# Kernel tuning notes

Measured on AMD Instinct MI355X. Metric: run time of the kernel, lower is better.

Reference implementation:

```python
import jax, jax.numpy as jnp
import numpy as np
import math

BS, CS, CT, H, W, HID = 32, 640, 768, 24, 24, 64
NUM_ITERS, REG = 50, 0.1


def setup_inputs() -> dict:
    key = jax.random.key(0)
    k1, k2, k3, k4, k5, k6 = jax.random.split(key, 6)
    feat_s = jax.random.normal(k1, (BS, CS, H, W), dtype=jnp.float32)
    feat_t = jax.random.normal(k2, (BS, CT, H, W), dtype=jnp.float32)
    Ws = jax.random.normal(k3, (HID, CS), dtype=jnp.float32) * (1.0 / math.sqrt(CS))
    bs = jax.random.normal(k4, (HID,), dtype=jnp.float32) * 0.01
    Wt = jax.random.normal(k5, (HID, CT), dtype=jnp.float32) * (1.0 / math.sqrt(CT))
    bt = jax.random.normal(k6, (HID,), dtype=jnp.float32) * 0.01
    return {"feat_s": feat_s, "feat_t": feat_t, "Ws": Ws, "bs": bs, "Wt": Wt, "bt": bt}


def _l2norm_dim1(x, eps=1e-12):
    # F.normalize(x, p=2, dim=1) on [BS, N, hid]: normalize over the TOKEN axis (dim=1)
    n = jnp.sqrt(jnp.sum(x * x, axis=1, keepdims=True))
    return x / jnp.maximum(n, eps)


def _log_otp_solver(log_a, log_b, M, num_iters, reg):
    Ms = M / reg  # [BS, N_s, N_t]
    u0 = jnp.zeros_like(log_a)
    v0 = jnp.zeros_like(log_b)

    def step(carry, _):
        u, v = carry
        u = log_a - jax.nn.logsumexp(Ms + v[:, None, :], axis=2)
        v = log_b - jax.nn.logsumexp(Ms + u[:, :, None], axis=1)
        return (u, v), None

    (u, v), _ = jax.lax.scan(step, (u0, v0), None, length=num_iters)
    return Ms + u[:, :, None] + v[:, None, :]


def _forward(feat_s, feat_t, Ws, bs, Wt, bt):
    B, Cs, h, w = feat_s.shape
    Ns = h * w
    B, Ct, ht, wt = feat_t.shape
    Nt = ht * wt
    xs = feat_s.reshape(B, Cs, Ns).transpose(0, 2, 1)  # [B, Ns, Cs]
    xt = feat_t.reshape(B, Ct, Nt).transpose(0, 2, 1)  # [B, Nt, Ct]
    # Linear + L2Norm(dim=1)
    xs = _l2norm_dim1(jnp.einsum('bnc,hc->bnh', xs, Ws) + bs)  # [B, Ns, hid]
    xt = _l2norm_dim1(jnp.einsum('bnc,hc->bnh', xt, Wt) + bt)  # [B, Nt, hid]
    # squared euclidean pairwise distances (cdist p=2, squared)
    sq_s = jnp.sum(xs * xs, axis=-1)  # [B, Ns]
    sq_t = jnp.sum(xt * xt, axis=-1)  # [B, Nt]
    dots = jnp.einsum('bnh,bmh->bnm', xs, xt)  # [B, Ns, Nt]
    M = jnp.maximum(sq_s[:, :, None] + sq_t[:, None, :] - 2.0 * dots, 0.0)
    log_a = jnp.full((B, Ns), -math.log(Ns), dtype=M.dtype)
    log_b = jnp.full((B, Nt), -math.log(Nt), dtype=M.dtype)
    log_T = _log_otp_solver(log_a, log_b, M, NUM_ITERS, REG)
    T = jnp.exp(log_T)
    return jnp.sum(T * M) / B


def reference(feat_s, feat_t, Ws, bs, Wt, bt):
    return _forward(feat_s, feat_t, Ws, bs, Wt, bt)
```

## Files before the change

### kernel.cpp

```cpp
#include <hip/hip_runtime.h>
#include <hip/hip_fp16.h>

#define BSZ 32
#define CS_ 640
#define CT_ 768
#define NTOK 576
#define HID 64
#define ITERS 50
#define WGB 8
#define ROWS 72
#define NWG (BSZ*WGB)
#define MPITCH 640
#define XPITCH 68

#define LOG2_N 9.169925001442312f
#define INV_N 0.001736111111111111f
#define MS_SCALE 14.426950408889634f
#define M_FROM_MSP 0.06931471805599453f

#define OFF_CNT 0
#define OFF_DONE 2048
#define OFF_GSUM 2056
#define OFF_DUMMY 2112
#define OFF_SQP 4160
#define OFF_PACC 151616
#define OFF_XS 299072
#define OFF_XT 2658368

#define L_MS 0
#define L_U 92160
#define L_V 92448
#define L_RED 95008
#define L_EUH 95072
#define L_MROW 95232
#define L_EWH 95520
#define L_UNION 96800
#define SMEM_BYTES 114048

typedef _Float16 half8 __attribute__((ext_vector_type(8)));
typedef _Float16 h2f __attribute__((ext_vector_type(2)));
typedef float f32x4 __attribute__((ext_vector_type(4)));

#if defined(__has_builtin)
#if __has_builtin(__builtin_amdgcn_fdot2)
#define HAVE_FDOT2 1
#endif
#endif

__device__ __forceinline__ float fdot2f(h2f a, h2f b, float c) {
#ifdef HAVE_FDOT2
    return __builtin_amdgcn_fdot2(a, b, c, false);
#else
    return fmaf((float)a[0], (float)b[0], fmaf((float)a[1], (float)b[1], c));
#endif
}

#define APITCH 40

template <int C>
__device__ __forceinline__ void proj_mfma(
    const float* __restrict__ feat,
    const float* __restrict__ W,
    const float* __restrict__ bias,
    __half* __restrict__ out,
    float* __restrict__ sqp,
    _Float16* lA, _Float16* lB, int nblk)
{
    const int tid = threadIdx.x;
    const int lane = tid & 63;
    const int wv = tid >> 6;
    const int n0 = nblk * 64;
    const int fr = lane & 15;
    const int kg = lane >> 4;

    f32x4 acc[4];
#pragma unroll
    for (int n = 0; n < 4; n++) acc[n] = (f32x4){0.f, 0.f, 0.f, 0.f};

    for (int c0 = 0; c0 < C; c0 += 32) {
        __syncthreads();
#pragma unroll
        for (int q = 0; q < 8; q++) {
            int idx = tid + q * 256;
            int t = idx & 63, c = idx >> 6;
            lA[t * APITCH + c] = (_Float16)feat[(size_t)(c0 + c) * NTOK + n0 + t];
        }
#pragma unroll
        for (int q = 0; q < 8; q++) {
            int idx = tid + q * 256;
            int c = idx & 31, h = idx >> 5;
            lB[h * APITCH + c] = (_Float16)W[(size_t)h * C + c0 + c];
        }
        __syncthreads();
        half8 a = *(const half8*)&lA[(wv * 16 + fr) * APITCH + kg * 8];
#pragma unroll
        for (int n = 0; n < 4; n++) {
            half8 b = *(const half8*)&lB[(n * 16 + fr) * APITCH + kg * 8];
            acc[n] = __builtin_amdgcn_mfma_f32_16x16x32_f16(a, b, acc[n], 0, 0, 0);
        }
    }

    __syncthreads();
    float* sred = (float*)lA;
#pragma unroll
    for (int n = 0; n < 4; n++) {
        const int h = n * 16 + fr;
        const float bv = bias[h];
        float s = 0.f;
#pragma unroll
        for (int reg = 0; reg < 4; reg++) {
            const int tok = wv * 16 + kg * 4 + reg;
            float val = acc[n][reg] + bv;
            out[(size_t)(n0 + tok) * HID + h] = __float2half(val);
            s = fmaf(val, val, s);
        }
        s += __shfl_xor(s, 16, 64);
        s += __shfl_xor(s, 32, 64);
        if (lane < 16) sred[wv * 64 + h] = s;
    }
    __syncthreads();
    if (tid < 64)
        sqp[tid] = sred[tid] + sred[64 + tid] + sred[128 + tid] + sred[192 + tid];
}

__global__ __launch_bounds__(256, 4) void k1_proj(
    const float* __restrict__ feat_s, const float* __restrict__ feat_t,
    const float* __restrict__ Ws, const float* __restrict__ bs,
    const float* __restrict__ Wt, const float* __restrict__ bt,
    __half* __restrict__ xs, __half* __restrict__ xt,
    float* __restrict__ sqpart, float* __restrict__ Pacc,
    int* __restrict__ counters, int* __restrict__ done, float* __restrict__ gsum)
{
    __shared__ __align__(16) _Float16 lA[64 * APITCH];
    __shared__ __align__(16) _Float16 lB[64 * APITCH];
    const int nblk = blockIdx.x, b = blockIdx.y, st = blockIdx.z;
    const int tid = threadIdx.x;

    if (st == 0 && nblk < 8) {
        float* pz = Pacc + (size_t)b * NTOK + nblk * 72;
        if (tid < 72) { pz[tid] = 0.f; pz[(size_t)BSZ * NTOK + tid] = 0.f; }
    }
    if (st == 1 && nblk == 0) {
        if (tid < 16) counters[b * 16 + tid] = 0;
        if (b == 0) {
            if (tid == 16) done[0] = 0;
            if (tid == 17) done[1] = 0;
            if (tid == 18) gsum[0] = 0.f;
        }
    }

    if (st == 0) {
        proj_mfma<CS_>(feat_s + (size_t)b * CS_ * NTOK, Ws, bs,
                       xs + (size_t)b * NTOK * HID,
                       sqpart + ((size_t)b * 9 + nblk) * 64, lA, lB, nblk);
    } else {
        proj_mfma<CT_>(feat_t + (size_t)b * CT_ * NTOK, Wt, bt,
                       xt + (size_t)b * NTOK * HID,
                       sqpart + ((size_t)(BSZ + b) * 9 + nblk) * 64, lA, lB, nblk);
    }
}

__global__ __launch_bounds__(1024, 8) void k4_sinkhorn(
    const __half* __restrict__ xsh, const __half* __restrict__ xth,
    const float* __restrict__ sqpart, float* __restrict__ Pacc,
    int* __restrict__ counters, int* __restrict__ done,
    float* __restrict__ gsum, float* __restrict__ dummyout,
    float* __restrict__ out)
{
    extern __shared__ char smem[];
    __half* Ms  = (__half*)(smem + L_MS);
    _Float16* MsH = (_Float16*)(smem + L_MS);
    float* u_l  = (float*)(smem + L_U);
    float* vlg  = (float*)(smem + L_V);
    float* red  = (float*)(smem + L_RED);
    _Float16* eu_h = (_Float16*)(smem + L_EUH);
    float* mrow = (float*)(smem + L_MROW);
    _Float16* ewh = (_Float16*)(smem + L_EWH);
    float* vtmp = (float*)(smem + L_UNION);
    float* ssc  = (float*)(smem + L_UNION);
    float* stc  = (float*)(smem + L_UNION + 256);
    float* sqs  = (float*)(smem + L_UNION + 512);
    float* sqt  = (float*)(smem + L_UNION + 800);
    __half* xs_l = (__half*)(smem + L_UNION + 3104);
    __half* xt_l = (__half*)(smem + L_UNION + 12896);

    const int tid = threadIdx.x;
    const int b = blockIdx.x & 31, part = blockIdx.x >> 5;
    const int r0 = part * ROWS;
    const int lane = tid & 63, wv = tid >> 6;
    float s_kept = 0.f;

    if (tid < 64) {
        const float* sp = sqpart + (size_t)b * 9 * 64 + tid;
        float s = 0.f;
#pragma unroll
        for (int k = 0; k < 9; k++) s += sp[k * 64];
        ssc[tid] = 1.0f / fmaxf(sqrtf(s), 1e-12f);
    } else if (tid < 128) {
        const float* sp = sqpart + (size_t)(BSZ + b) * 9 * 64 + (tid - 64);
        float s = 0.f;
#pragma unroll
        for (int k = 0; k < 9; k++) s += sp[k * 64];
        stc[tid - 64] = 1.0f / fmaxf(sqrtf(s), 1e-12f);
    }
    for (int m = tid; m < MPITCH; m += 1024) ewh[m] = (m < NTOK) ? (_Float16)1.0f : (_Float16)0.0f;
    __syncthreads();

    for (int idx = tid; idx < ROWS * 64; idx += 1024) {
        int r = idx >> 6, h = idx & 63;
        xs_l[r * XPITCH + h] =
            __float2half(__half2float(xsh[((size_t)b * NTOK + r0 + r) * 64 + h]) * ssc[h]);
    }
    if (tid < NTOK) {
        const __half* tp = xth + ((size_t)b * NTOK + tid) * 64;
        float s = 0.f;
#pragma unroll
        for (int h = 0; h < 64; h++) { float v = __half2float(tp[h]) * stc[h]; s = fmaf(v, v, s); }
        sqt[tid] = s;
    }
    __syncthreads();
    if (tid < ROWS) {
        float s = 0.f;
#pragma unroll
        for (int h = 0; h < 64; h++) { float v = __half2float(xs_l[tid * XPITCH + h]); s = fmaf(v, v, s); }
        sqs[tid] = s;
    }

    for (int c0 = 0; c0 < NTOK; c0 += 32) {
        __syncthreads();
        for (int idx = tid; idx < 32 * 64; idx += 1024) {
            int m = idx >> 6, h = idx & 63;
            xt_l[m * XPITCH + h] =
                __float2half(__half2float(xth[((size_t)b * NTOK + c0 + m) * 64 + h]) * stc[h]);
        }
        __syncthreads();
        for (int idx = tid; idx < ROWS * 32; idx += 1024) {
            int r = idx >> 5, c = idx & 31;
            const __half2* xr = (const __half2*)(xs_l + r * XPITCH);
            const __half2* tr = (const __half2*)(xt_l + c * XPITCH);
            float d = 0.f;
#pragma unroll
            for (int h2 = 0; h2 < 32; h2++) {
                float2 av = __half22float2(xr[h2]);
                float2 tv = __half22float2(tr[h2]);
                d = fmaf(av.x, tv.x, d);
                d = fmaf(av.y, tv.y, d);
            }
            float M = fmaxf(sqs[r] + sqt[c] - 2.f * d, 0.f);
            Ms[r * MPITCH + c0 + c] = __float2half(M * MS_SCALE);
        }
    }
    __syncthreads();
    for (int idx = tid; idx < ROWS * (MPITCH - NTOK); idx += 1024) {
        int r = idx >> 6, k = idx & 63;
        Ms[r * MPITCH + NTOK + k] = __float2half(-1000.f);
    }
    __syncthreads();

    for (int r = wv; r < ROWS; r += 16) {
        __half* row = Ms + r * MPITCH;
        float2 f[5];
        float mx = 0.f;
#pragma unroll
        for (int j = 0; j < 5; j++) {
            f[j] = __half22float2(*(const __half2*)&row[128 * j + 2 * lane]);
            mx = fmaxf(mx, fmaxf(f[j].x, f[j].y));
        }
#pragma unroll
        for (int off = 32; off > 0; off >>= 1) mx = fmaxf(mx, __shfl_xor(mx, off, 64));
        if (lane == 0) mrow[r] = mx;
#pragma unroll
        for (int j = 0; j < 5; j++) {
            *(__half2*)&row[128 * j + 2 * lane] = __floats2half2_rn(
                __builtin_amdgcn_exp2f(f[j].x - mx), __builtin_amdgcn_exp2f(f[j].y - mx));
        }
    }
    __syncthreads();

    int* flags = counters + b * 16;

    for (int it = 1; it <= ITERS; ++it) {
        if (it > 1) {
            if (tid < NTOK) {
                const int qr = (it - 1) & 1, qw = it & 1;
                float s = __hip_atomic_load(&Pacc[(size_t)(qr * BSZ + b) * NTOK + tid],
                                            __ATOMIC_RELAXED, __HIP_MEMORY_SCOPE_AGENT);
                ewh[tid] = (_Float16)(INV_N * __builtin_amdgcn_rcpf(s));
                if (tid >= r0 && tid < r0 + ROWS) {
                    if (s_kept != 0.f)
                        (void)__hip_atomic_fetch_add(
                            &Pacc[(size_t)(qw * BSZ + b) * NTOK + tid], -s_kept,
                            __ATOMIC_RELAXED, __HIP_MEMORY_SCOPE_AGENT);
                    s_kept = s;
                }
            }
            __syncthreads();
        }
        h2f vrh[5];
#pragma unroll
        for (int j = 0; j < 5; j++) vrh[j] = *(const h2f*)&ewh[128 * j + 2 * lane];
        for (int r = wv; r < ROWS; r += 16) {
            const _Float16* row = MsH + r * MPITCH;
            float a = 0.f;
#pragma unroll
            for (int j = 0; j < 5; j++)
                a = fdot2f(*(const h2f*)&row[128 * j + 2 * lane], vrh[j], a);
#pragma unroll
            for (int off = 32; off > 0; off >>= 1) a += __shfl_xor(a, off, 64);
            if (lane == 0) {
                eu_h[r] = (_Float16)(INV_N * __builtin_amdgcn_rcpf(a));
                u_l[r] = -LOG2_N - __builtin_amdgcn_logf(a);
            }
        }
        __syncthreads();
        if (tid < 864) {
            int q = tid / 288, p = tid - q * 288;
            const _Float16* col = MsH + 2 * p;
            float a0 = 0.f, a1 = 0.f;
            int n1 = q * 24;
#pragma unroll
            for (int nn = 0; nn < 12; nn++, n1 += 2) {
                uint ea = *(const uint*)&col[n1 * MPITCH];
                uint eb = *(const uint*)&col[(n1 + 1) * MPITCH];
                h2f up = *(const h2f*)&eu_h[n1];
                uint xpk = __builtin_amdgcn_perm(eb, ea, 0x05040100u);
                uint ypk = __builtin_amdgcn_perm(eb, ea, 0x07060302u);
                a0 = fdot2f(__builtin_bit_cast(h2f, xpk), up, a0);
                a1 = fdot2f(__builtin_bit_cast(h2f, ypk), up, a1);
            }
            ((float2*)(vtmp + q * NTOK))[p] = make_float2(a0, a1);
        }
        __syncthreads();
        if (tid < NTOK) {
            float s = vtmp[tid] + vtmp[NTOK + tid] + vtmp[2 * NTOK + tid];
            (void)__hip_atomic_fetch_add(&Pacc[(size_t)((it & 1) * BSZ + b) * NTOK + tid], s,
                                         __ATOMIC_RELAXED, __HIP_MEMORY_SCOPE_AGENT);
        }
        __syncthreads();
        if (tid < WGB) {
            if (tid == part)
                __hip_atomic_store(&flags[tid], it, __ATOMIC_RELAXED, __HIP_MEMORY_SCOPE_AGENT);
            while (__hip_atomic_load(&flags[tid], __ATOMIC_RELAXED, __HIP_MEMORY_SCOPE_AGENT) < it)
                __builtin_amdgcn_s_sleep(1);
        }
        __syncthreads();
    }

    if (tid < NTOK) {
        float s = __hip_atomic_load(&Pacc[(size_t)b * NTOK + tid],
                                    __ATOMIC_RELAXED, __HIP_MEMORY_SCOPE_AGENT);
        vlg[tid] = -LOG2_N - __builtin_amdgcn_logf(s);
    }
    __syncthreads();
    float acc = 0.f;
    for (int idx = tid; idx < ROWS * NTOK; idx += 1024) {
        int r = idx / NTOK, m = idx - r * NTOK;
        float e = __half2float(Ms[r * MPITCH + m]);
        if (e > 0.f) {
            float msp = __builtin_amdgcn_logf(e) + mrow[r];
            acc = fmaf(__builtin_amdgcn_exp2f(u_l[r] + vlg[m]) * e, msp, acc);
        }
    }
#pragma unroll
    for (int off = 32; off > 0; off >>= 1) acc += __shfl_xor(acc, off, 64);
    if (lane == 0) red[wv] = acc;
    __syncthreads();
    if (tid == 0) {
        float s = 0.f;
#pragma unroll
        for (int w2 = 0; w2 < 16; w2++) s += red[w2];
        float old = __hip_atomic_fetch_add(gsum, s * M_FROM_MSP,
                                           __ATOMIC_RELAXED, __HIP_MEMORY_SCOPE_AGENT);
        int* dptr = done + ((old == -1.2345678e33f) ? 1 : 0);
        int prev = __hip_atomic_fetch_add(dptr, 1, __ATOMIC_RELAXED, __HIP_MEMORY_SCOPE_AGENT);
        if (prev == NWG - 1) {
            float tot = __hip_atomic_load(gsum, __ATOMIC_RELAXED, __HIP_MEMORY_SCOPE_AGENT);
            out[0] = tot * (1.0f / BSZ);
        }
        if (old == -1.2345678e33f) dummyout[blockIdx.x] = 1.f;
    }
}

extern "C" void kernel_launch(void* const* d_in, const int* in_sizes, int n_in,
                              void* d_out, int out_size, void* d_ws, size_t ws_size,
                              hipStream_t stream) {
    const float* feat_s = (const float*)d_in[0];
    const float* feat_t = (const float*)d_in[1];
    const float* Ws = (const float*)d_in[2];
    const float* bs = (const float*)d_in[3];
    const float* Wt = (const float*)d_in[4];
    const float* bt = (const float*)d_in[5];

    char* ws = (char*)d_ws;
    int* counters  = (int*)(ws + OFF_CNT);
    int* done      = (int*)(ws + OFF_DONE);
    float* gsum    = (float*)(ws + OFF_GSUM);
    float* dummyo  = (float*)(ws + OFF_DUMMY);
    float* sqpart  = (float*)(ws + OFF_SQP);
    float* Pacc    = (float*)(ws + OFF_PACC);
    __half* xs     = (__half*)(ws + OFF_XS);
    __half* xt     = (__half*)(ws + OFF_XT);
    float* out = (float*)d_out;


    hipLaunchKernelGGL(k1_proj, dim3(9, 32, 2), dim3(256), 0, stream,
                       feat_s, feat_t, Ws, bs, Wt, bt, xs, xt,
                       sqpart, Pacc, counters, done, gsum);

    (void)hipFuncSetAttribute((const void*)k4_sinkhorn,
                              hipFuncAttributeMaxDynamicSharedMemorySize, SMEM_BYTES);
    hipLaunchKernelGGL(k4_sinkhorn, dim3(NWG), dim3(1024), SMEM_BYTES, stream,
                       xs, xt, sqpart, Pacc, counters, done, gsum, dummyo, out);
}
```

Baseline: 406.1 us.

## Fuse row and column Sinkhorn passes into single sweep over Ms tile

Measured after the change: 392.8 us. 1.03x faster.

```diff
diff --git a/kernel.cpp b/kernel.cpp
--- a/kernel.cpp
+++ b/kernel.cpp
@@ -12,6 +12,7 @@
 #define NWG (BSZ*WGB)
 #define MPITCH 640
 #define XPITCH 68
+#define VTP 644
 
 #define LOG2_N 9.169925001442312f
 #define INV_N 0.001736111111111111f
@@ -31,11 +32,11 @@
 #define L_U 92160
 #define L_V 92448
 #define L_RED 95008
-#define L_EUH 95072
-#define L_MROW 95232
-#define L_EWH 95520
-#define L_UNION 96800
-#define SMEM_BYTES 114048
+#define L_MROW 95072
+#define L_EWH 95360
+#define L_VT 96640
+#define L_UNION L_VT
+#define SMEM_BYTES 137856
 
 typedef _Float16 half8 __attribute__((ext_vector_type(8)));
 typedef _Float16 h2f __attribute__((ext_vector_type(2)));
@@ -160,7 +161,7 @@
     }
 }
 
-__global__ __launch_bounds__(1024, 8) void k4_sinkhorn(
+__global__ __launch_bounds__(1024, 4) void k4_sinkhorn(
     const __half* __restrict__ xsh, const __half* __restrict__ xth,
     const float* __restrict__ sqpart, float* __restrict__ Pacc,
     int* __restrict__ counters, int* __restrict__ done,
@@ -173,10 +174,9 @@
     float* u_l  = (float*)(smem + L_U);
     float* vlg  = (float*)(smem + L_V);
     float* red  = (float*)(smem + L_RED);
-    _Float16* eu_h = (_Float16*)(smem + L_EUH);
     float* mrow = (float*)(smem + L_MROW);
     _Float16* ewh = (_Float16*)(smem + L_EWH);
-    float* vtmp = (float*)(smem + L_UNION);
+    float* vtmp = (float*)(smem + L_VT);
     float* ssc  = (float*)(smem + L_UNION);
     float* stc  = (float*)(smem + L_UNION + 256);
     float* sqs  = (float*)(smem + L_UNION + 512);
@@ -299,40 +299,41 @@
         h2f vrh[5];
 #pragma unroll
         for (int j = 0; j < 5; j++) vrh[j] = *(const h2f*)&ewh[128 * j + 2 * lane];
+        float2 colacc[5];
+#pragma unroll
+        for (int j = 0; j < 5; j++) colacc[j] = make_float2(0.f, 0.f);
+
         for (int r = wv; r < ROWS; r += 16) {
             const _Float16* row = MsH + r * MPITCH;
+            uint e[5];
             float a = 0.f;
 #pragma unroll
+            for (int j = 0; j < 5; j++) {
+                e[j] = *(const uint*)&row[128 * j + 2 * lane];
+                a = fdot2f(__builtin_bit_cast(h2f, e[j]), vrh[j], a);
+            }
+#pragma unroll
+            for (int off = 32; off > 0; off >>= 1) a += __shfl_xor(a, off, 64);
+            float eu = INV_N * __builtin_amdgcn_rcpf(a);
+            if (lane == 0) u_l[r] = -LOG2_N - __builtin_amdgcn_logf(a);
+#pragma unroll
+            for (int j = 0; j < 5; j++) {
+                float2 f = __half22float2(__builtin_bit_cast(__half2, e[j]));
+                colacc[j].x = fmaf(f.x, eu, colacc[j].x);
+                colacc[j].y = fmaf(f.y, eu, colacc[j].y);
+            }
+        }
+        {
+            float* vt = vtmp + wv * VTP;
+#pragma unroll
             for (int j = 0; j < 5; j++)
-                a = fdot2f(*(const h2f*)&row[128 * j + 2 * lane], vrh[j], a);
-#pragma unroll
-            for (int off = 32; off > 0; off >>= 1) a += __shfl_xor(a, off, 64);
-            if (lane == 0) {
-                eu_h[r] = (_Float16)(INV_N * __builtin_amdgcn_rcpf(a));
-                u_l[r] = -LOG2_N - __builtin_amdgcn_logf(a);
-            }
-        }
-        __syncthreads();
-        if (tid < 864) {
-            int q = tid / 288, p = tid - q * 288;
-            const _Float16* col = MsH + 2 * p;
-            float a0 = 0.f, a1 = 0.f;
-            int n1 = q * 24;
-#pragma unroll
-            for (int nn = 0; nn < 12; nn++, n1 += 2) {
-                uint ea = *(const uint*)&col[n1 * MPITCH];
-                uint eb = *(const uint*)&col[(n1 + 1) * MPITCH];
-                h2f up = *(const h2f*)&eu_h[n1];
-                uint xpk = __builtin_amdgcn_perm(eb, ea, 0x05040100u);
-                uint ypk = __builtin_amdgcn_perm(eb, ea, 0x07060302u);
-                a0 = fdot2f(__builtin_bit_cast(h2f, xpk), up, a0);
-                a1 = fdot2f(__builtin_bit_cast(h2f, ypk), up, a1);
-            }
-            ((float2*)(vtmp + q * NTOK))[p] = make_float2(a0, a1);
+                *(float2*)&vt[128 * j + 2 * lane] = colacc[j];
         }
         __syncthreads();
         if (tid < NTOK) {
-            float s = vtmp[tid] + vtmp[NTOK + tid] + vtmp[2 * NTOK + tid];
+            float s = 0.f;
+#pragma unroll
+            for (int w = 0; w < 16; w++) s += vtmp[w * VTP + tid];
             (void)__hip_atomic_fetch_add(&Pacc[(size_t)((it & 1) * BSZ + b) * NTOK + tid], s,
                                          __ATOMIC_RELAXED, __HIP_MEMORY_SCOPE_AGENT);
         }
```
